# Performance work log

Hardware: AMD Instinct MI355X
Metric: run time of the kernel (lower is better)

Reference implementation:

```python
import jax, jax.numpy as jnp
import numpy as np

KNN = 5
MAX_STEPS = 100
LAM = 1.0  # bound_lambda


def setup_inputs() -> dict:
    key = jax.random.key(0)
    k1, k2 = jax.random.split(key)
    # probabilities in (0,1): softmax-like scores
    scores_raw = jax.random.uniform(k1, (1, 8192, 8, 8), dtype=jnp.float32)
    feats = jax.random.normal(k2, (1, 8192, 256, 1, 1), dtype=jnp.float32)
    return {"scores_raw": scores_raw, "feats": feats}


def knn_affinity(X, knn):
    # X: (N, D) L2-normalized features. Same math as torch.norm(x_i - x_j):
    # ||xi-xj|| = sqrt(|xi|^2 + |xj|^2 - 2 xi.xj), avoids the O(N^2 D) broadcast.
    N = X.shape[0]
    sq = jnp.sum(X * X, axis=-1)                                  # (N,)
    dist2 = sq[:, None] + sq[None, :] - 2.0 * (X @ X.T)           # (N, N)
    dist = jnp.sqrt(jnp.maximum(dist2, 0.0))
    n_neighbors = min(knn + 1, N)
    _, idx = jax.lax.top_k(-dist, n_neighbors)                    # smallest distances
    idx = idx[:, 1:]                                              # drop self
    W = jnp.zeros((N, N), X.dtype).at[jnp.arange(N)[:, None], idx].set(1.0)
    return W


def reference(scores_raw, feats):
    _, _, H, W = scores_raw.shape
    unary = -jnp.log(scores_raw.reshape(-1, H * W) + 1e-10)       # (N, K)
    f = feats.reshape(feats.shape[0], feats.shape[1], -1)[0]       # (N, D), flatten(-3).squeeze(0)
    nrm = jnp.linalg.norm(f, axis=-1, keepdims=True)
    f = f / jnp.maximum(nrm, 1e-12)                                # F.normalize(p=2)
    kernel = knn_affinity(f, KNN)                                  # (N, N)

    Y0 = jax.nn.softmax(-unary, axis=-1)

    def cond(state):
        i, Y, oldE, conv = state
        return (i < MAX_STEPS) & (~conv)

    def body(state):
        i, Y, oldE, _ = state
        pairwise = LAM * (kernel @ Y)                              # (N, K)
        Ynew = jax.nn.softmax(-unary + pairwise, axis=-1)
        # entropy_energy (note: lambda multiplies pairwise again, as in source)
        E = jnp.sum(unary * Ynew - LAM * pairwise * Ynew
                    + Ynew * jnp.log(jnp.clip(Ynew, 1e-20)))
        conv = (i > 1) & (jnp.abs(E - oldE) <= 1e-8 * jnp.abs(oldE))
        return (i + 1, Ynew, E, conv)

    init = (jnp.int32(0), Y0, jnp.float32(jnp.inf), jnp.bool_(False))
    _, Y, _, _ = jax.lax.while_loop(cond, body, init)
    return Y
```

## Files before the change

kernel.cpp:

```cpp
#include <hip/hip_runtime.h>
#include <math.h>

#define NROWS 8192
#define DIM   256
#define NCLS  64
#define KNN   5
#define NCAND 8
#define NSPLIT 4
#define MAXSTEPS 100
#define PBLK 256

struct GS {
  double Eold;
  double Epart[PBLK];
  int pad0[30];
  int gcnt[16 * 32];
  int root; int pad1[31];
  int gen;  int pad2[31];
  int flag; int pad3[31];
};

typedef __attribute__((ext_vector_type(8))) short bf16x8;
typedef __attribute__((ext_vector_type(4))) float f32x4;

typedef __attribute__((address_space(1))) unsigned int glb_u32_t;
typedef __attribute__((address_space(3))) unsigned int lds_u32_t;
__device__ __forceinline__ void async_cp16(const uint4* g, uint4* l) {
  __builtin_amdgcn_global_load_lds((const glb_u32_t*)(const unsigned int*)g,
                                   (lds_u32_t*)(unsigned int*)l, 16, 0, 0);
}

__device__ __forceinline__ float aloadf(const float* p) {
  return __hip_atomic_load(p, __ATOMIC_RELAXED, __HIP_MEMORY_SCOPE_AGENT);
}
__device__ __forceinline__ void astoref(float* p, float v) {
  __hip_atomic_store(p, v, __ATOMIC_RELAXED, __HIP_MEMORY_SCOPE_AGENT);
}
__device__ __forceinline__ double aloadd(const double* p) {
  return __hip_atomic_load(p, __ATOMIC_RELAXED, __HIP_MEMORY_SCOPE_AGENT);
}
__device__ __forceinline__ void astored(double* p, double v) {
  __hip_atomic_store(p, v, __ATOMIC_RELAXED, __HIP_MEMORY_SCOPE_AGENT);
}
__device__ __forceinline__ int aloadi(const int* p) {
  return __hip_atomic_load(p, __ATOMIC_RELAXED, __HIP_MEMORY_SCOPE_AGENT);
}
__device__ __forceinline__ void astorei(int* p, int v) {
  __hip_atomic_store(p, v, __ATOMIC_RELAXED, __HIP_MEMORY_SCOPE_AGENT);
}
__device__ __forceinline__ int afetchadd(int* p) {
  return __hip_atomic_fetch_add(p, 1, __ATOMIC_RELAXED, __HIP_MEMORY_SCOPE_AGENT);
}

__device__ __forceinline__ float wave_sum64(float v) {
#pragma unroll
  for (int m = 32; m >= 1; m >>= 1) v += __shfl_xor(v, m, 64);
  return v;
}
__device__ __forceinline__ double wave_sum64d(double v) {
#pragma unroll
  for (int m = 32; m >= 1; m >>= 1) v += __shfl_xor(v, m, 64);
  return v;
}

__device__ __forceinline__ unsigned short f2bf(float x) {
  unsigned u = __float_as_uint(x);
  u += 0x7FFFu + ((u >> 16) & 1u);
  return (unsigned short)(u >> 16);
}

__device__ __forceinline__ void cs_desc(unsigned& a, unsigned& b) {
  unsigned hi = a > b ? a : b;
  unsigned lo = a > b ? b : a;
  a = hi; b = lo;
}

__global__ void k_normalize(const float* __restrict__ feats, uint2* __restrict__ fb2,
                            float* __restrict__ f, double* __restrict__ sqd) {
  int row  = blockIdx.x * 4 + (threadIdx.x >> 6);
  int lane = threadIdx.x & 63;
  float4 v = ((const float4*)(feats + (size_t)row * DIM))[lane];
  double ss = (double)v.x * v.x + (double)v.y * v.y + (double)v.z * v.z + (double)v.w * v.w;
  ss = wave_sum64d(ss);
  float nr = fmaxf((float)sqrt(ss), 1e-12f);
  float4 o;
  o.x = v.x / nr; o.y = v.y / nr; o.z = v.z / nr; o.w = v.w / nr;
  ((float4*)(f + (size_t)row * DIM))[lane] = o;
  double s2 = (double)o.x * o.x + (double)o.y * o.y + (double)o.z * o.z + (double)o.w * o.w;
  s2 = wave_sum64d(s2);
  if (lane == 0) sqd[row] = s2;
  uint2 w2;
  w2.x = (unsigned)f2bf(o.x) | ((unsigned)f2bf(o.y) << 16);
  w2.y = (unsigned)f2bf(o.z) | ((unsigned)f2bf(o.w) << 16);
  int T = row >> 6, rl = row & 63, g = lane >> 1, h = lane & 1;
  fb2[((size_t)T * 2048 + rl * 32 + (g ^ (rl & 31))) * 2 + h] = w2;
}

#define JSPAN (NROWS / NSPLIT)
#define GT2 (JSPAN / 32)

__launch_bounds__(256, 4)
__global__ void k_gram(const uint4* __restrict__ fb, int* __restrict__ candp) {
  __shared__ uint4 Bsh4[2][1024];

  const int t = threadIdx.x;
  const int L   = (blockIdx.x & 7) * 128 + (blockIdx.x >> 3);
  const int js  = L >> 8;
  const int ib2 = L & 255;
  const int i0 = ib2 * 32;
  const int jbase = js * JSPAN;
  const int w = t >> 6, lane = t & 63;
  const int s = w & 1, si = w >> 1;
  const int m15 = lane & 15, quad = lane >> 4;

  const size_t abase = (size_t)(ib2 >> 1) * 2048 + (size_t)(ib2 & 1) * 1024;

  {
    const uint4* At = fb + abase;
    const uint4* Bt = fb + (size_t)(js * 32) * 2048;
#pragma unroll
    for (int p = 0; p < 4; ++p) {
      int c = w * 4 + p;
      async_cp16(At + c * 64 + lane, &Bsh4[1][c * 64]);
      async_cp16(Bt + c * 64 + lane, &Bsh4[0][c * 64]);
    }
  }
  __syncthreads();

  bf16x8 areg[8];
  {
    int lr = s * 16 + m15;
#pragma unroll
    for (int kc = 0; kc < 8; ++kc)
      areg[kc] = ((const bf16x8*)Bsh4[1])[lr * 32 + ((kc * 4 + quad) ^ (lr & 31))];
  }
  __syncthreads();

  unsigned mk[NCAND];
#pragma unroll
  for (int k = 0; k < NCAND; ++k) mk[k] = 0u;
  float thr = -1e30f;

  for (int jt = 0; jt < GT2; ++jt) {
    const int cbuf = jt & 1;
    if (jt > 0) __syncthreads();
    if (jt + 1 < GT2) {
      const int jn = jt + 1;
      const uint4* Bt = fb + (size_t)(js * 32 + (jn >> 1)) * 2048 + (size_t)(jn & 1) * 1024;
#pragma unroll
      for (int p = 0; p < 4; ++p) {
        int c = w * 4 + p;
        async_cp16(Bt + c * 64 + lane, &Bsh4[1 - cbuf][c * 64]);
      }
    }

    f32x4 acc = (f32x4)(0.f);
#pragma unroll
    for (int kc = 0; kc < 8; ++kc) {
      int rb = si * 16 + m15;
      bf16x8 bv = ((const bf16x8*)Bsh4[cbuf])[rb * 32 + ((kc * 4 + quad) ^ (rb & 31))];
      acc = __builtin_amdgcn_mfma_f32_16x16x32_bf16(bv, areg[kc], acc, 0, 0, 0);
    }

    {
      float g4 = fmaxf(fmaxf(acc[0], acc[1]), fmaxf(acc[2], acc[3]));
      if (g4 > thr) {
        const unsigned cbase = (unsigned)(jt * 32 + si * 16 + quad * 4);
        unsigned n[4];
#pragma unroll
        for (int e = 0; e < 4; ++e) {
          unsigned ub = __float_as_uint(acc[e]);
          n[e] = ((ub ^ (unsigned)(((int)ub >> 31) | 0x80000000)) & ~2047u)
                 | (cbase + (unsigned)e);
        }
        cs_desc(n[0], n[1]); cs_desc(n[2], n[3]);
        cs_desc(n[0], n[2]); cs_desc(n[1], n[3]);
        cs_desc(n[1], n[2]);
        unsigned m[8];
        m[0] = mk[0]; m[1] = mk[1]; m[2] = mk[2]; m[3] = mk[3];
        m[4] = mk[4] > n[3] ? mk[4] : n[3];
        m[5] = mk[5] > n[2] ? mk[5] : n[2];
        m[6] = mk[6] > n[1] ? mk[6] : n[1];
        m[7] = mk[7] > n[0] ? mk[7] : n[0];
        cs_desc(m[0], m[4]); cs_desc(m[1], m[5]); cs_desc(m[2], m[6]); cs_desc(m[3], m[7]);
        cs_desc(m[0], m[2]); cs_desc(m[1], m[3]); cs_desc(m[4], m[6]); cs_desc(m[5], m[7]);
        cs_desc(m[0], m[1]); cs_desc(m[2], m[3]); cs_desc(m[4], m[5]); cs_desc(m[6], m[7]);
#pragma unroll
        for (int i = 0; i < 8; ++i) mk[i] = m[i];
        unsigned kb = mk[NCAND - 1] & ~2047u;
        if (kb) {
          unsigned xm = 0x80000000u | ~(unsigned)((int)kb >> 31);
          thr = __uint_as_float(kb ^ xm);
        }
      }
    }
  }

  __syncthreads();
  unsigned* Ksh = (unsigned*)Bsh4;
  {
    int row = s * 16 + m15;
    int slot0 = (si * 4 + quad) * 8;
#pragma unroll
    for (int k = 0; k < NCAND; ++k)
      Ksh[row * 64 + ((slot0 + k + row) & 63)] = mk[k];
  }
  __syncthreads();
  if (t < 32) {
    unsigned fk[NCAND];
#pragma unroll
    for (int k = 0; k < NCAND; ++k) fk[k] = 0u;
    for (int ss = 0; ss < 64; ++ss) {
      unsigned kk = Ksh[t * 64 + ((ss + t) & 63)];
      if (kk > fk[NCAND - 1]) {
        fk[NCAND - 1] = kk;
#pragma unroll
        for (int q = NCAND - 1; q >= 1; --q)
          if (fk[q] > fk[q - 1]) { unsigned tm = fk[q]; fk[q] = fk[q - 1]; fk[q - 1] = tm; }
      }
    }
#pragma unroll
    for (int k = 0; k < NCAND; ++k)
      candp[(size_t)js * (NROWS * NCAND) + (size_t)(i0 + t) * NCAND + k] =
          jbase + (int)(fk[k] & 2047u);
  }
}

__global__ void k_refine(const float* __restrict__ f, const double* __restrict__ sqd,
                         const int* __restrict__ candp, int* __restrict__ nbr) {
  const int row = blockIdx.x * 4 + (threadIdx.x >> 6);
  const int t = threadIdx.x & 63;
  const int c = t >> 1;
  const int seg = t & 1;
  const int split = c >> 3, slot = c & 7;
  int j = candp[(size_t)split * (NROWS * NCAND) + (size_t)row * NCAND + slot];
  const float4* fi4 = (const float4*)(f + (size_t)row * DIM) + seg * 32;
  const float4* fj4 = (const float4*)(f + (size_t)j * DIM) + seg * 32;
  double dot = 0.0;
#pragma unroll 8
  for (int d4 = 0; d4 < 32; ++d4) {
    float4 a = fi4[d4], b = fj4[d4];
    dot = fma((double)a.x, (double)b.x, dot);
    dot = fma((double)a.y, (double)b.y, dot);
    dot = fma((double)a.z, (double)b.z, dot);
    dot = fma((double)a.w, (double)b.w, dot);
  }
  dot += __shfl_xor(dot, 1, 64);
  double key = sqd[j] - 2.0 * dot;
  bool valid = (seg == 0) && (j != row);
  for (int s = 0; s < KNN; ++s) {
    double v = valid ? key : (double)INFINITY;
    int vj = valid ? j : 0x7fffffff;
#pragma unroll
    for (int m = 1; m < 64; m <<= 1) {
      double ov = __shfl_xor(v, m, 64);
      int oj = __shfl_xor(vj, m, 64);
      if (ov < v || (ov == v && oj < vj)) { v = ov; vj = oj; }
    }
    if (valid && vj == j) valid = false;
    if (t == 0) nbr[(size_t)row * 8 + s] = vj;
  }
}

__global__ void k_solve(const float* __restrict__ scores,
                        const int* __restrict__ nbr,
                        float* __restrict__ Ya, float* __restrict__ Yb,
                        float* __restrict__ out, GS* __restrict__ gs) {
  const int b = blockIdx.x;
  const int w = threadIdx.x >> 6, lane = threadIdx.x & 63;
  const int row0 = b * 32 + w * 4;
  const int grp = (b & 15) * 32;
  __shared__ int nbl[32][5];
  __shared__ double sE[8];
  __shared__ int sflag;

  if (threadIdx.x < 160)
    nbl[threadIdx.x / 5][threadIdx.x % 5] =
        nbr[(size_t)(b * 32 + threadIdx.x / 5) * 8 + (threadIdx.x % 5)];

  float u[4], y[4];
#pragma unroll
  for (int r = 0; r < 4; ++r)
    u[r] = -logf(scores[(size_t)(row0 + r) * NCLS + lane] + 1e-10f);
#pragma unroll
  for (int r = 0; r < 4; ++r) {
    float e = expf(-u[r]);
    float sum = wave_sum64(e);
    y[r] = e / sum;
    astoref(&Ya[(size_t)(row0 + r) * NCLS + lane], y[r]);
  }
  __syncthreads();

  int nboff[4][KNN];
#pragma unroll
  for (int r = 0; r < 4; ++r)
#pragma unroll
    for (int k = 0; k < KNN; ++k)
      nboff[r][k] = nbl[w * 4 + r][k] * NCLS + lane;

  int mygen = 1;
  if (threadIdx.x == 0) {
    __builtin_amdgcn_fence(__ATOMIC_RELEASE, "workgroup");
    int old = afetchadd(&gs->gcnt[grp]);
    if (old == 15) {
      int r = afetchadd(&gs->root);
      if (r == 15) {
#pragma unroll
        for (int m = 0; m < 16; ++m) astorei(&gs->gcnt[m * 32], 0);
        astorei(&gs->root, 0);
        __builtin_amdgcn_fence(__ATOMIC_RELEASE, "workgroup");
        astorei(&gs->gen, mygen);
      }
    }
    while (aloadi(&gs->gen) < mygen) __builtin_amdgcn_s_sleep(1);
  }
  __syncthreads();
  ++mygen;

  for (int iter = 0; iter < MAXSTEPS; ++iter) {
    const float* __restrict__ Yin = (iter & 1) ? Yb : Ya;
    float* __restrict__ Yout = (iter & 1) ? Ya : Yb;
    double ew = 0.0;
#pragma unroll
    for (int r = 0; r < 4; ++r) {
      float pw = 0.f;
#pragma unroll
      for (int k = 0; k < KNN; ++k) pw += aloadf(&Yin[nboff[r][k]]);
      float e = expf(pw - u[r]);
      float sum = wave_sum64(e);
      y[r] = e / sum;
      astoref(&Yout[(size_t)(row0 + r) * NCLS + lane], y[r]);
      ew += -(double)logf(sum);
    }
    if (lane == 0) sE[w] = ew;
    __syncthreads();
    if (w == 0) {
      double be = (lane < 8) ? sE[lane] : 0.0;
      be = wave_sum64d(be);
      int last = 0;
      if (lane == 0) {
        astored(&gs->Epart[b], be);
        __builtin_amdgcn_fence(__ATOMIC_RELEASE, "workgroup");
        int old = afetchadd(&gs->gcnt[grp]);
        if (old == 15) {
          int r = afetchadd(&gs->root);
          last = (r == 15);
        }
      }
      last = __shfl(last, 0, 64);
      if (last) {
        double s = 0.0;
#pragma unroll
        for (int i = 0; i < 4; ++i) s += aloadd(&gs->Epart[lane + 64 * i]);
        s = wave_sum64d(s);
        if (lane < 16) astorei(&gs->gcnt[lane * 32], 0);
        if (lane == 0) {
          astorei(&gs->root, 0);
          double eo = aloadd(&gs->Eold);
          int conv = (iter > 1) && (fabs(s - eo) <= 1e-8 * fabs(eo));
          astorei(&gs->flag, conv);
          if (!conv) astored(&gs->Eold, s);
        }
        __builtin_amdgcn_fence(__ATOMIC_RELEASE, "workgroup");
        if (lane == 0) astorei(&gs->gen, mygen);
      }
      if (lane == 0) {
        while (aloadi(&gs->gen) < mygen) __builtin_amdgcn_s_sleep(1);
        sflag = aloadi(&gs->flag);
      }
    }
    __syncthreads();
    ++mygen;
    if (sflag) break;
  }

#pragma unroll
  for (int r = 0; r < 4; ++r)
    out[(size_t)(row0 + r) * NCLS + lane] = y[r];
}

__global__ void k_init(GS* gs) {
  int t = threadIdx.x;
  if (t == 0) {
    gs->Eold = (double)INFINITY;
    gs->root = 0; gs->gen = 0; gs->flag = 0;
  }
  if (t < 16 * 32) gs->gcnt[t] = 0;
}

extern "C" void kernel_launch(void* const* d_in, const int* in_sizes, int n_in,
                              void* d_out, int out_size, void* d_ws, size_t ws_size,
                              hipStream_t stream) {
  (void)in_sizes; (void)n_in; (void)out_size; (void)ws_size;
  const float* scores = (const float*)d_in[0];
  const float* feats  = (const float*)d_in[1];
  float* out = (float*)d_out;
  char* ws = (char*)d_ws;
  uint4*  fb    = (uint4*)(ws + 0);
  float*  f     = (float*)(ws + 4194304);
  float*  Ya    = (float*)(ws + 4194304);
  float*  Yb    = (float*)(ws + 6291456);
  double* sqd   = (double*)(ws + 12582912);
  int*    candp = (int*)(ws + 12648448);
  int*    nbr   = (int*)(ws + 13697024);
  GS*     gs    = (GS*)(ws + 13959168);

  k_init<<<1, 512, 0, stream>>>(gs);
  k_normalize<<<NROWS / 4, 256, 0, stream>>>(feats, (uint2*)fb, f, sqd);
  k_gram<<<(NROWS / 32) * NSPLIT, 256, 0, stream>>>(fb, candp);
  k_refine<<<NROWS / 4, 256, 0, stream>>>(f, sqd, candp, nbr);
  k_solve<<<PBLK, 512, 0, stream>>>(scores, nbr, Ya, Yb, out, gs);
}
```

Measured before the change: 235.8 us.

## Enlarge gram tile to 64x64 with 512 threads and register-blocked A rows

The kNN gram kernel now processes 64 query rows per block against 64-column B tiles using 8 waves. Each wave holds two 16-row A fragments and reuses each loaded B fragment for two MFMAs. This halves the number of B tile loads per output and the grid size, aiming to cut LDS and global traffic in the distance phase. In exchange it doubles LDS use and register pressure, and the final merge is serialized over 128 candidates per row on 64 threads.

```diff
diff --git a/kernel.cpp b/kernel.cpp
--- a/kernel.cpp
+++ b/kernel.cpp
@@ -97,26 +97,24 @@
 }
 
 #define JSPAN (NROWS / NSPLIT)
-#define GT2 (JSPAN / 32)
-
-__launch_bounds__(256, 4)
+#define GTILES (JSPAN / 64)
+
+__launch_bounds__(512, 4)
 __global__ void k_gram(const uint4* __restrict__ fb, int* __restrict__ candp) {
-  __shared__ uint4 Bsh4[2][1024];
-
-  const int t = threadIdx.x;
-  const int L   = (blockIdx.x & 7) * 128 + (blockIdx.x >> 3);
-  const int js  = L >> 8;
-  const int ib2 = L & 255;
-  const int i0 = ib2 * 32;
+  __shared__ uint4 Bsh4[2][2048];
+
+  const int t  = threadIdx.x;
+  const int ib = blockIdx.x >> 2;
+  const int js = blockIdx.x & 3;
+  const int i0 = ib * 64;
   const int jbase = js * JSPAN;
   const int w = t >> 6, lane = t & 63;
-  const int s = w & 1, si = w >> 1;
+  const int ap = w >> 2;
+  const int sb = w & 3;
   const int m15 = lane & 15, quad = lane >> 4;
 
-  const size_t abase = (size_t)(ib2 >> 1) * 2048 + (size_t)(ib2 & 1) * 1024;
-
   {
-    const uint4* At = fb + abase;
+    const uint4* At = fb + (size_t)ib * 2048;
     const uint4* Bt = fb + (size_t)(js * 32) * 2048;
 #pragma unroll
     for (int p = 0; p < 4; ++p) {
@@ -127,26 +125,30 @@
   }
   __syncthreads();
 
-  bf16x8 areg[8];
-  {
-    int lr = s * 16 + m15;
+  bf16x8 areg[2][8];
+#pragma unroll
+  for (int st = 0; st < 2; ++st) {
+    int ra = ap * 32 + st * 16 + m15;
 #pragma unroll
     for (int kc = 0; kc < 8; ++kc)
-      areg[kc] = ((const bf16x8*)Bsh4[1])[lr * 32 + ((kc * 4 + quad) ^ (lr & 31))];
-  }
-  __syncthreads();
-
-  unsigned mk[NCAND];
-#pragma unroll
-  for (int k = 0; k < NCAND; ++k) mk[k] = 0u;
-  float thr = -1e30f;
-
-  for (int jt = 0; jt < GT2; ++jt) {
+      areg[st][kc] = ((const bf16x8*)Bsh4[1])[ra * 32 + ((kc * 4 + quad) ^ (ra & 31))];
+  }
+  __syncthreads();
+
+  unsigned mk[2][NCAND];
+#pragma unroll
+  for (int st = 0; st < 2; ++st)
+#pragma unroll
+    for (int k = 0; k < NCAND; ++k) mk[st][k] = 0u;
+  float thr[2] = {-1e30f, -1e30f};
+
+  const int rb = sb * 16 + m15;
+
+  for (int jt = 0; jt < GTILES; ++jt) {
     const int cbuf = jt & 1;
     if (jt > 0) __syncthreads();
-    if (jt + 1 < GT2) {
-      const int jn = jt + 1;
-      const uint4* Bt = fb + (size_t)(js * 32 + (jn >> 1)) * 2048 + (size_t)(jn & 1) * 1024;
+    if (jt + 1 < GTILES) {
+      const uint4* Bt = fb + (size_t)(js * 32 + jt + 1) * 2048;
 #pragma unroll
       for (int p = 0; p < 4; ++p) {
         int c = w * 4 + p;
@@ -154,22 +156,25 @@
       }
     }
 
-    f32x4 acc = (f32x4)(0.f);
+    f32x4 acc[2];
+    acc[0] = (f32x4)(0.f); acc[1] = (f32x4)(0.f);
 #pragma unroll
     for (int kc = 0; kc < 8; ++kc) {
-      int rb = si * 16 + m15;
       bf16x8 bv = ((const bf16x8*)Bsh4[cbuf])[rb * 32 + ((kc * 4 + quad) ^ (rb & 31))];
-      acc = __builtin_amdgcn_mfma_f32_16x16x32_bf16(bv, areg[kc], acc, 0, 0, 0);
-    }
-
-    {
-      float g4 = fmaxf(fmaxf(acc[0], acc[1]), fmaxf(acc[2], acc[3]));
-      if (g4 > thr) {
-        const unsigned cbase = (unsigned)(jt * 32 + si * 16 + quad * 4);
+      acc[0] = __builtin_amdgcn_mfma_f32_16x16x32_bf16(bv, areg[0][kc], acc[0], 0, 0, 0);
+      acc[1] = __builtin_amdgcn_mfma_f32_16x16x32_bf16(bv, areg[1][kc], acc[1], 0, 0, 0);
+    }
+
+    const unsigned cbase = (unsigned)(jt * 64 + sb * 16 + quad * 4);
+#pragma unroll
+    for (int st = 0; st < 2; ++st) {
+      f32x4 v = acc[st];
+      float g4 = fmaxf(fmaxf(v[0], v[1]), fmaxf(v[2], v[3]));
+      if (g4 > thr[st]) {
         unsigned n[4];
 #pragma unroll
         for (int e = 0; e < 4; ++e) {
-          unsigned ub = __float_as_uint(acc[e]);
+          unsigned ub = __float_as_uint(v[e]);
           n[e] = ((ub ^ (unsigned)(((int)ub >> 31) | 0x80000000)) & ~2047u)
                  | (cbase + (unsigned)e);
         }
@@ -177,20 +182,20 @@
         cs_desc(n[0], n[2]); cs_desc(n[1], n[3]);
         cs_desc(n[1], n[2]);
         unsigned m[8];
-        m[0] = mk[0]; m[1] = mk[1]; m[2] = mk[2]; m[3] = mk[3];
-        m[4] = mk[4] > n[3] ? mk[4] : n[3];
-        m[5] = mk[5] > n[2] ? mk[5] : n[2];
-        m[6] = mk[6] > n[1] ? mk[6] : n[1];
-        m[7] = mk[7] > n[0] ? mk[7] : n[0];
+        m[0] = mk[st][0]; m[1] = mk[st][1]; m[2] = mk[st][2]; m[3] = mk[st][3];
+        m[4] = mk[st][4] > n[3] ? mk[st][4] : n[3];
+        m[5] = mk[st][5] > n[2] ? mk[st][5] : n[2];
+        m[6] = mk[st][6] > n[1] ? mk[st][6] : n[1];
+        m[7] = mk[st][7] > n[0] ? mk[st][7] : n[0];
         cs_desc(m[0], m[4]); cs_desc(m[1], m[5]); cs_desc(m[2], m[6]); cs_desc(m[3], m[7]);
         cs_desc(m[0], m[2]); cs_desc(m[1], m[3]); cs_desc(m[4], m[6]); cs_desc(m[5], m[7]);
         cs_desc(m[0], m[1]); cs_desc(m[2], m[3]); cs_desc(m[4], m[5]); cs_desc(m[6], m[7]);
 #pragma unroll
-        for (int i = 0; i < 8; ++i) mk[i] = m[i];
-        unsigned kb = mk[NCAND - 1] & ~2047u;
+        for (int i = 0; i < 8; ++i) mk[st][i] = m[i];
+        unsigned kb = mk[st][NCAND - 1] & ~2047u;
         if (kb) {
           unsigned xm = 0x80000000u | ~(unsigned)((int)kb >> 31);
-          thr = __uint_as_float(kb ^ xm);
+          thr[st] = __uint_as_float(kb ^ xm);
         }
       }
     }
@@ -198,20 +203,21 @@
 
   __syncthreads();
   unsigned* Ksh = (unsigned*)Bsh4;
-  {
-    int row = s * 16 + m15;
-    int slot0 = (si * 4 + quad) * 8;
+#pragma unroll
+  for (int st = 0; st < 2; ++st) {
+    int row = ap * 32 + st * 16 + m15;
+    int slot0 = (sb * 4 + quad) * 8;
 #pragma unroll
     for (int k = 0; k < NCAND; ++k)
-      Ksh[row * 64 + ((slot0 + k + row) & 63)] = mk[k];
-  }
-  __syncthreads();
-  if (t < 32) {
+      Ksh[row * 128 + ((slot0 + k + row) & 127)] = mk[st][k];
+  }
+  __syncthreads();
+  if (t < 64) {
     unsigned fk[NCAND];
 #pragma unroll
     for (int k = 0; k < NCAND; ++k) fk[k] = 0u;
-    for (int ss = 0; ss < 64; ++ss) {
-      unsigned kk = Ksh[t * 64 + ((ss + t) & 63)];
+    for (int ss = 0; ss < 128; ++ss) {
+      unsigned kk = Ksh[t * 128 + ((ss + t) & 127)];
       if (kk > fk[NCAND - 1]) {
         fk[NCAND - 1] = kk;
 #pragma unroll
@@ -407,7 +413,7 @@
 
   k_init<<<1, 512, 0, stream>>>(gs);
   k_normalize<<<NROWS / 4, 256, 0, stream>>>(feats, (uint2*)fb, f, sqd);
-  k_gram<<<(NROWS / 32) * NSPLIT, 256, 0, stream>>>(fb, candp);
+  k_gram<<<(NROWS / 64) * NSPLIT, 512, 0, stream>>>(fb, candp);
   k_refine<<<NROWS / 4, 256, 0, stream>>>(f, sqd, candp, nbr);
   k_solve<<<PBLK, 512, 0, stream>>>(scores, nbr, Ya, Yb, out, gs);
 }
```

After: 228.9 us. 1.03x faster.
